# Performance work log

Hardware: AMD Instinct MI355X
Metric: run time of the kernel (lower is better)

The kernel has to match this reference:

```python
import jax, jax.numpy as jnp
import numpy as np


def _dgs_sample(feat, gxy):
    """Bilinear sample + analytic spatial derivatives.
    feat: [b,h,w,c]; gxy: [b,q,2] normalized coords in [-1,1] (align_corners=True,
    zero padding outside). Returns phi, phi_on_i (d/d grid_y), phi_on_j (d/d grid_x),
    each [b,q,c].
    """
    b, h, w, c = feat.shape
    gx = gxy[..., 0]
    gy = gxy[..., 1]
    jx = (gx + 1.0) * (0.5 * (w - 1))  # pixel x (column j)
    iy = (gy + 1.0) * (0.5 * (h - 1))  # pixel y (row i)
    j0f = jnp.floor(jx)
    i0f = jnp.floor(iy)
    tx = (jx - j0f)[..., None]  # [b,q,1]
    ty = (iy - i0f)[..., None]
    j0 = j0f.astype(jnp.int32)
    i0 = i0f.astype(jnp.int32)
    feat_flat = feat.reshape(b, h * w, c)

    def gather(ii, jj):
        valid = (ii >= 0) & (ii < h) & (jj >= 0) & (jj < w)
        idx = jnp.clip(ii, 0, h - 1) * w + jnp.clip(jj, 0, w - 1)
        g = jnp.take_along_axis(feat_flat, idx[:, :, None], axis=1)  # [b,q,c]
        return g * valid[:, :, None].astype(feat.dtype)

    g00 = gather(i0, j0)
    g01 = gather(i0, j0 + 1)
    g10 = gather(i0 + 1, j0)
    g11 = gather(i0 + 1, j0 + 1)

    phi = (1.0 - ty) * ((1.0 - tx) * g00 + tx * g01) + ty * ((1.0 - tx) * g10 + tx * g11)
    dphi_djx = (1.0 - ty) * (g01 - g00) + ty * (g11 - g10)      # d/d pixel-x
    dphi_diy = (1.0 - tx) * (g10 - g00) + tx * (g11 - g01)      # d/d pixel-y
    # chain rule back to normalized grid coordinates
    phi_on_j = dphi_djx * (0.5 * (w - 1))
    phi_on_i = dphi_diy * (0.5 * (h - 1))
    return phi, phi_on_i, phi_on_j


def setup_inputs() -> dict:
    key = jax.random.key(0)
    k1, k2, k3, k4, k5 = jax.random.split(key, 5)
    b, c, h, w, q = 4, 32, 512, 512, 65536
    inp = jax.random.normal(k1, (b, c, h, w), dtype=jnp.float32)
    xy = jax.random.uniform(k2, (b, q, 2), dtype=jnp.float32, minval=-0.95, maxval=0.95)
    z = jax.random.uniform(k3, (b, q, 1), dtype=jnp.float32, minval=0.5, maxval=1.5)
    grid = jnp.concatenate([xy, z], axis=2)  # pCamPersp [b,q,3]
    fScaleWidth = jax.random.uniform(k4, (b,), dtype=jnp.float32, minval=0.8, maxval=1.2)
    fScaleHeight = jax.random.uniform(k5, (b,), dtype=jnp.float32, minval=0.8, maxval=1.2)
    return {"input": inp, "grid": grid, "fScaleWidth": fScaleWidth, "fScaleHeight": fScaleHeight}


def reference(input, grid, fScaleWidth, fScaleHeight):
    # input: [b,c,h,w]; grid (pCamPersp): [b,q,3]; fScale*: [b]
    feat = jnp.transpose(input, (0, 2, 3, 1))  # [b,h,w,c]
    phi, phi_on_i, phi_on_j = _dgs_sample(feat, grid[:, :, :2])  # [b,q,c]
    # permute to [b,c,q] as in the torch wrapper
    phi = jnp.transpose(phi, (0, 2, 1))
    phi_on_i = jnp.transpose(phi_on_i, (0, 2, 1))
    phi_on_j = jnp.transpose(phi_on_j, (0, 2, 1))

    z = jax.lax.stop_gradient(grid[:, :, 2])          # [b,q]
    x = jax.lax.stop_gradient(grid[:, :, 0])
    y = jax.lax.stop_gradient(grid[:, :, 1])
    fh_over_z = fScaleHeight[:, None] / z
    fw_over_z = fScaleWidth[:, None] / z
    y_over_z = y / z
    x_over_z = x / z

    phi_on_xCam = phi_on_j * fw_over_z[:, None, :]
    phi_on_yCam = phi_on_i * fh_over_z[:, None, :]
    phi_on_zCam = -phi_on_i * y_over_z[:, None, :] - phi_on_j * x_over_z[:, None, :]
    # [b, c, 4, q]
    return jnp.stack([phi, phi_on_xCam, phi_on_yCam, phi_on_zCam], axis=2)
```

## Files before the change

kernel.cpp:

```cpp
#include <hip/hip_runtime.h>

constexpr int B = 4, C = 32, H = 512, W = 512, Q = 65536;
constexpr int CP = 4;
constexpr int NCHUNK = C / CP;
constexpr int NXCD = 8;
constexpr size_t PLANE = (size_t)H * W;
constexpr size_t WS_NEED = (size_t)B * NCHUNK * PLANE * 8 + 16;

__device__ __forceinline__ unsigned short f2bf(float f) {
    unsigned u = __float_as_uint(f);
    u += 0x7fffu + ((u >> 16) & 1u);
    return (unsigned short)(u >> 16);
}
__device__ __forceinline__ float bf2f(unsigned short s) {
    return __uint_as_float((unsigned)s << 16);
}

struct __attribute__((packed, aligned(8))) row8 { unsigned short u[8]; };

__global__ __launch_bounds__(256) void interleave_kernel(
    const float* __restrict__ input, ushort4* __restrict__ ws)
{
    int t = blockIdx.x * 256 + (int)threadIdx.x;
    int px = t & (int)(PLANE - 1);
    int pr = t >> 18;
    int b = pr >> 3, chunk = pr & 7;
    const float* p = input + ((size_t)b * C + chunk * CP) * PLANE + px;
    ushort4 v;
    v.x = f2bf(p[0]);
    v.y = f2bf(p[PLANE]);
    v.z = f2bf(p[2 * PLANE]);
    v.w = f2bf(p[3 * PLANE]);
    ws[(size_t)pr * PLANE + px] = v;
}

__global__ __launch_bounds__(256) void dgs_gather(
    const ushort4* __restrict__ ws,
    const float* __restrict__ grid,
    const float* __restrict__ fsw,
    const float* __restrict__ fsh,
    float* __restrict__ out)
{
    int bid = blockIdx.x;
    int xcd  = bid & (NXCD - 1);
    int slot = bid >> 3;
    int pair = xcd + NXCD * (slot >> 8);
    int qblk = slot & 255;
    int chunk = pair >> 2;
    int b     = pair & 3;
    int q = (qblk << 8) | (int)threadIdx.x;

    const float* g3 = grid + (size_t)(b * Q + q) * 3;
    float gx = g3[0];
    float gy = g3[1];
    float gz = g3[2];

    const float sx = 0.5f * (float)(W - 1);
    const float sy = 0.5f * (float)(H - 1);
    float jx = (gx + 1.0f) * sx;
    float iy = (gy + 1.0f) * sy;
    float j0f = floorf(jx);
    float i0f = floorf(iy);
    float tx = jx - j0f;
    float ty = iy - i0f;
    int j0 = (int)j0f;
    int i0 = (int)i0f;
    int j1 = j0 + 1, i1 = i0 + 1;

    float m00 = (i0 >= 0 && i0 < H && j0 >= 0 && j0 < W) ? 1.f : 0.f;
    float m01 = (i0 >= 0 && i0 < H && j1 >= 0 && j1 < W) ? 1.f : 0.f;
    float m10 = (i1 >= 0 && i1 < H && j0 >= 0 && j0 < W) ? 1.f : 0.f;
    float m11 = (i1 >= 0 && i1 < H && j1 >= 0 && j1 < W) ? 1.f : 0.f;
    int i0c = min(max(i0, 0), H - 1), i1c = min(max(i1, 0), H - 1);
    int j0c = min(max(j0, 0), W - 1);

    const ushort4* wp = ws + (size_t)(b * NCHUNK + chunk) * PLANE;
    row8 v0 = *reinterpret_cast<const row8*>(wp + i0c * W + j0c);
    row8 v1 = *reinterpret_cast<const row8*>(wp + i1c * W + j0c);

    float fw = fsw[b];
    float fh = fsh[b];
    float inv_z = 1.0f / gz;
    float fw_over_z = fw * inv_z;
    float fh_over_z = fh * inv_z;
    float x_over_z = gx * inv_z;
    float y_over_z = gy * inv_z;

    float omtx = 1.0f - tx, omty = 1.0f - ty;

    const int cg0 = chunk * CP;
    float* ob = out + ((size_t)(b * C + cg0) * 4) * Q + q;

    #pragma unroll
    for (int c = 0; c < CP; ++c) {
        float g00 = bf2f(v0.u[c])     * m00;
        float g01 = bf2f(v0.u[c + 4]) * m01;
        float g10 = bf2f(v1.u[c])     * m10;
        float g11 = bf2f(v1.u[c + 4]) * m11;

        float top = g00 * omtx + g01 * tx;
        float bot = g10 * omtx + g11 * tx;
        float phi = top * omty + bot * ty;
        float dphi_djx = (g01 - g00) * omty + (g11 - g10) * ty;
        float dphi_diy = (g10 - g00) * omtx + (g11 - g01) * tx;
        float phi_on_j = dphi_djx * sx;
        float phi_on_i = dphi_diy * sy;

        float* o = ob + (size_t)c * 4 * Q;
        __builtin_nontemporal_store(phi, o);
        __builtin_nontemporal_store(phi_on_j * fw_over_z, o + (size_t)Q);
        __builtin_nontemporal_store(phi_on_i * fh_over_z, o + (size_t)2 * Q);
        __builtin_nontemporal_store(-phi_on_i * y_over_z - phi_on_j * x_over_z,
                                    o + (size_t)3 * Q);
    }
}

struct __attribute__((packed, aligned(4))) f2pair { float x, y; };

__global__ __launch_bounds__(256) void dgs_kernel(
    const float* __restrict__ input, const float* __restrict__ grid,
    const float* __restrict__ fsw, const float* __restrict__ fsh,
    float* __restrict__ out)
{
    int bid = blockIdx.x;
    int xcd  = bid & (NXCD - 1);
    int slot = bid >> 3;
    int pair = xcd + NXCD * (slot >> 8);
    int qblk = slot & 255;
    int chunk = pair >> 2;
    int b     = pair & 3;
    int q = (qblk << 8) | (int)threadIdx.x;

    const float* g3 = grid + (size_t)(b * Q + q) * 3;
    float gx = g3[0], gy = g3[1], gz = g3[2];
    const float sx = 0.5f * (float)(W - 1);
    const float sy = 0.5f * (float)(H - 1);
    float jx = (gx + 1.0f) * sx;
    float iy = (gy + 1.0f) * sy;
    float j0f = floorf(jx), i0f = floorf(iy);
    float tx = jx - j0f, ty = iy - i0f;
    int j0 = (int)j0f, i0 = (int)i0f;
    int j1 = j0 + 1, i1 = i0 + 1;
    float m00 = (i0 >= 0 && i0 < H && j0 >= 0 && j0 < W) ? 1.f : 0.f;
    float m01 = (i0 >= 0 && i0 < H && j1 >= 0 && j1 < W) ? 1.f : 0.f;
    float m10 = (i1 >= 0 && i1 < H && j0 >= 0 && j0 < W) ? 1.f : 0.f;
    float m11 = (i1 >= 0 && i1 < H && j1 >= 0 && j1 < W) ? 1.f : 0.f;
    int i0c = min(max(i0, 0), H - 1), i1c = min(max(i1, 0), H - 1);
    int j0c = min(max(j0, 0), W - 1);
    int off00 = i0c * W + j0c;
    int off10 = i1c * W + j0c;
    float fw = fsw[b], fh = fsh[b];
    float inv_z = 1.0f / gz;
    float fw_over_z = fw * inv_z, fh_over_z = fh * inv_z;
    float x_over_z = gx * inv_z, y_over_z = gy * inv_z;
    float omtx = 1.0f - tx, omty = 1.0f - ty;
    const int cg0 = chunk * CP;
    const float* inb = input + ((size_t)b * C + cg0) * PLANE;
    float* ob = out + ((size_t)(b * C + cg0) * 4) * Q + q;
    #pragma unroll
    for (int c = 0; c < CP; ++c) {
        const float* p = inb + (size_t)c * PLANE;
        f2pair v0 = *reinterpret_cast<const f2pair*>(p + off00);
        f2pair v1 = *reinterpret_cast<const f2pair*>(p + off10);
        float g00 = v0.x * m00, g01 = v0.y * m01;
        float g10 = v1.x * m10, g11 = v1.y * m11;
        float top = g00 * omtx + g01 * tx;
        float bot = g10 * omtx + g11 * tx;
        float phi = top * omty + bot * ty;
        float dphi_djx = (g01 - g00) * omty + (g11 - g10) * ty;
        float dphi_diy = (g10 - g00) * omtx + (g11 - g01) * tx;
        float phi_on_j = dphi_djx * sx;
        float phi_on_i = dphi_diy * sy;
        float* o = ob + (size_t)c * 4 * Q;
        o[0]             = phi;
        o[(size_t)Q]     = phi_on_j * fw_over_z;
        o[(size_t)2 * Q] = phi_on_i * fh_over_z;
        o[(size_t)3 * Q] = -phi_on_i * y_over_z - phi_on_j * x_over_z;
    }
}

extern "C" void kernel_launch(void* const* d_in, const int* in_sizes, int n_in,
                              void* d_out, int out_size, void* d_ws, size_t ws_size,
                              hipStream_t stream) {
    const float* input = (const float*)d_in[0];
    const float* grid  = (const float*)d_in[1];
    const float* fsw   = (const float*)d_in[2];
    const float* fsh   = (const float*)d_in[3];
    float* out = (float*)d_out;

    if (ws_size >= WS_NEED) {
        ushort4* ws = (ushort4*)d_ws;
        int t1 = B * NCHUNK * (int)PLANE;
        hipLaunchKernelGGL(interleave_kernel, dim3(t1 / 256), dim3(256), 0,
                           stream, input, ws);
        int t2 = B * Q * NCHUNK;
        hipLaunchKernelGGL(dgs_gather, dim3(t2 / 256), dim3(256), 0, stream,
                           ws, grid, fsw, fsh, out);
    } else {
        int total = B * Q * NCHUNK;
        hipLaunchKernelGGL(dgs_kernel, dim3(total / 256), dim3(256), 0, stream,
                           input, grid, fsw, fsh, out);
    }
}
```

Baseline: 69.23 us.

## Vectorize interleave kernel with XCD-aware mapping and reverse gather plane order for L2 reuse

The bf16 interleave kernel now has each thread process four pixels using 16-byte nontemporal loads per channel, and launches 8192 blocks instead of one thread per pixel. Blocks are mapped so that each XCD writes the same (batch, chunk) planes its gather blocks later read. The gather kernel walks the planes in reverse order, so the planes written last by the interleave pass (likely still in cache) are read first. Workspace indexing switches to a pair-major layout, which the two kernels must agree on.

```diff
diff --git a/kernel.cpp b/kernel.cpp
--- a/kernel.cpp
+++ b/kernel.cpp
@@ -7,6 +7,8 @@
 constexpr size_t PLANE = (size_t)H * W;
 constexpr size_t WS_NEED = (size_t)B * NCHUNK * PLANE * 8 + 16;
 
+typedef float vfloat4 __attribute__((ext_vector_type(4)));
+
 __device__ __forceinline__ unsigned short f2bf(float f) {
     unsigned u = __float_as_uint(f);
     u += 0x7fffu + ((u >> 16) & 1u);
@@ -21,17 +23,26 @@
 __global__ __launch_bounds__(256) void interleave_kernel(
     const float* __restrict__ input, ushort4* __restrict__ ws)
 {
-    int t = blockIdx.x * 256 + (int)threadIdx.x;
-    int px = t & (int)(PLANE - 1);
-    int pr = t >> 18;
-    int b = pr >> 3, chunk = pr & 7;
-    const float* p = input + ((size_t)b * C + chunk * CP) * PLANE + px;
-    ushort4 v;
-    v.x = f2bf(p[0]);
-    v.y = f2bf(p[PLANE]);
-    v.z = f2bf(p[2 * PLANE]);
-    v.w = f2bf(p[3 * PLANE]);
-    ws[(size_t)pr * PLANE + px] = v;
+    int bid = blockIdx.x;
+    int xcd  = bid & (NXCD - 1);
+    int slot = bid >> 3;
+    int pair = xcd + NXCD * (slot >> 8);
+    int slice = slot & 255;
+    int b = pair & 3, chunk = pair >> 2;
+
+    int px0 = (slice << 10) | ((int)threadIdx.x << 2);
+    const float* p = input + ((size_t)b * C + chunk * CP) * PLANE + px0;
+
+    vfloat4 f0 = __builtin_nontemporal_load(reinterpret_cast<const vfloat4*>(p));
+    vfloat4 f1 = __builtin_nontemporal_load(reinterpret_cast<const vfloat4*>(p + PLANE));
+    vfloat4 f2 = __builtin_nontemporal_load(reinterpret_cast<const vfloat4*>(p + 2 * PLANE));
+    vfloat4 f3 = __builtin_nontemporal_load(reinterpret_cast<const vfloat4*>(p + 3 * PLANE));
+
+    ushort4* wp = ws + (size_t)pair * PLANE + px0;
+    wp[0] = { f2bf(f0.x), f2bf(f1.x), f2bf(f2.x), f2bf(f3.x) };
+    wp[1] = { f2bf(f0.y), f2bf(f1.y), f2bf(f2.y), f2bf(f3.y) };
+    wp[2] = { f2bf(f0.z), f2bf(f1.z), f2bf(f2.z), f2bf(f3.z) };
+    wp[3] = { f2bf(f0.w), f2bf(f1.w), f2bf(f2.w), f2bf(f3.w) };
 }
 
 __global__ __launch_bounds__(256) void dgs_gather(
@@ -44,7 +55,7 @@
     int bid = blockIdx.x;
     int xcd  = bid & (NXCD - 1);
     int slot = bid >> 3;
-    int pair = xcd + NXCD * (slot >> 8);
+    int pair = xcd + NXCD * (3 - (slot >> 8));
     int qblk = slot & 255;
     int chunk = pair >> 2;
     int b     = pair & 3;
@@ -74,7 +85,7 @@
     int i0c = min(max(i0, 0), H - 1), i1c = min(max(i1, 0), H - 1);
     int j0c = min(max(j0, 0), W - 1);
 
-    const ushort4* wp = ws + (size_t)(b * NCHUNK + chunk) * PLANE;
+    const ushort4* wp = ws + (size_t)pair * PLANE;
     row8 v0 = *reinterpret_cast<const row8*>(wp + i0c * W + j0c);
     row8 v1 = *reinterpret_cast<const row8*>(wp + i1c * W + j0c);
 
@@ -190,8 +201,7 @@
 
     if (ws_size >= WS_NEED) {
         ushort4* ws = (ushort4*)d_ws;
-        int t1 = B * NCHUNK * (int)PLANE;
-        hipLaunchKernelGGL(interleave_kernel, dim3(t1 / 256), dim3(256), 0,
+        hipLaunchKernelGGL(interleave_kernel, dim3(8192), dim3(256), 0,
                            stream, input, ws);
         int t2 = B * Q * NCHUNK;
         hipLaunchKernelGGL(dgs_gather, dim3(t2 / 256), dim3(256), 0, stream,
```

Measured after the change: 73.58 us. 1.06x slower.
